# Kernel tuning notes

Hardware: AMD Instinct MI355X
Metric: run time of the kernel (lower is better)

The kernel has to match this reference:

```python
import jax, jax.numpy as jnp
import numpy as np

# --- static config ---
B = 64        # graphs per batch
NPG = 512     # nodes per graph
N = B * NPG   # total nodes = 32768
EPG = 8192    # edges per graph (avg degree 16)
E = B * EPG   # total edges = 524288
L = 16        # tokens per node
V = 50000     # vocab
H = 256       # hidden_size == rnn hidden_size
P = 128       # projection_dim
K1 = 256      # ceil(0.5 * 512) nodes kept after pool 1
K2 = 128      # ceil(0.5 * 256) nodes kept after pool 2
PAD = 0


def setup_inputs() -> dict:
    key = jax.random.key(0)
    ks = jax.random.split(key, 16)
    tokens = jax.random.randint(ks[0], (N, L), 0, V, dtype=jnp.int32)
    eg = jnp.repeat(jnp.arange(B, dtype=jnp.int32), EPG)  # graph id per edge
    src = jax.random.randint(ks[1], (E,), 0, NPG, dtype=jnp.int32) + eg * NPG
    dst = jax.random.randint(ks[2], (E,), 0, NPG, dtype=jnp.int32) + eg * NPG
    edge_attr = jax.random.uniform(ks[3], (E, 2), dtype=jnp.float32)
    sH = 1.0 / np.sqrt(H).astype(np.float32)
    sP = 1.0 / np.sqrt(P).astype(np.float32)
    return {
        'tokens': tokens, 'src': src, 'dst': dst, 'edge_attr': edge_attr,
        'emb': jax.random.normal(ks[4], (V, H), jnp.float32) * 0.05,
        'W0': jax.random.normal(ks[5], (H, H), jnp.float32) * sH,
        'b0': jnp.zeros((H,), jnp.float32),
        'W1': jax.random.normal(ks[6], (H, H), jnp.float32) * sH,
        'b1': jnp.zeros((H,), jnp.float32),
        'p0': jax.random.normal(ks[7], (H,), jnp.float32),
        'p1': jax.random.normal(ks[8], (H,), jnp.float32),
        'wg': jax.random.normal(ks[9], (H, 1), jnp.float32) * sH,
        'bg': jnp.zeros((1,), jnp.float32),
        'Wp1': jax.random.normal(ks[10], (H, P), jnp.float32) * sH,
        'bp1': jnp.zeros((P,), jnp.float32),
        'Wp2': jax.random.normal(ks[11], (P, P), jnp.float32) * sP,
        'bp2': jnp.zeros((P,), jnp.float32),
    }


def _st_encode(tokens, emb):
    # STEncoder proxy: embed token ids, masked mean over non-pad tokens -> [N, H]
    mask = (tokens != PAD).astype(jnp.float32)  # [N, L]
    e = emb[tokens] * mask[..., None]           # [N, L, H]
    cnt = jnp.maximum(mask.sum(-1, keepdims=True), 1.0)
    return e.sum(1) / cnt


def _gcn(x, W, b, src, dst, w, n):
    # GCNConv with edge weights + self loops (fill 1), symmetric normalization
    h = x @ W                                        # [n, H]
    deg = jax.ops.segment_sum(w, dst, num_segments=n) + 1.0
    dinv = jax.lax.rsqrt(deg)
    norm = dinv[src] * w * dinv[dst]                 # [E]
    agg = jax.ops.segment_sum(h[src] * norm[:, None], dst, num_segments=n)
    return agg + h * (1.0 / deg)[:, None] + b


def _topk_pool(x, p, src, dst, w, n_per, k):
    # TopKPooling: score = x.p/||p||, keep top-k per graph, gate by tanh(score)
    G = x.shape[0] // n_per
    score = (x @ p) / jnp.linalg.norm(p)
    vals, idx = jax.lax.top_k(score.reshape(G, n_per), k)   # [G, k]
    perm = (idx + (jnp.arange(G, dtype=jnp.int32) * n_per)[:, None]).reshape(-1)
    x_new = x[perm] * jnp.tanh(vals.reshape(-1))[:, None]
    new_of_old = jnp.full((G * n_per,), -1, jnp.int32).at[perm].set(
        jnp.arange(G * k, dtype=jnp.int32))
    ns, nd = new_of_old[src], new_of_old[dst]
    keep = (ns >= 0) & (nd >= 0)
    # masked edges: weight 0 -> contribute nothing (== subgraph filtering)
    return (x_new, jnp.where(keep, ns, 0), jnp.where(keep, nd, 0),
            jnp.where(keep, w, 0.0))


def _attpool(x, wg, bg, k):
    # GlobalAttention: softmax(Linear(x,1)) over each graph's nodes
    G = x.shape[0] // k
    gate = (x @ wg + bg).reshape(G, k)        # [G, k]
    a = jax.nn.softmax(gate, axis=1)
    return jnp.einsum('gk,gkh->gh', a, x.reshape(G, k, x.shape[-1]))


def reference(tokens, src, dst, edge_attr, emb, W0, b0, W1, b1, p0, p1,
              wg, bg, Wp1, bp1, Wp2, bp2):
    w = edge_attr.mean(axis=1)                 # GCN path: scalar edge weights
    x = _st_encode(tokens, emb)                # [N, H]
    # layer 1
    x = jax.nn.relu(_gcn(x, W0, b0, src, dst, w, N))
    x, src1, dst1, w1 = _topk_pool(x, p0, src, dst, w, NPG, K1)
    out = _attpool(x, wg, bg, K1)              # [B, H]
    # hidden layer
    x = jax.nn.relu(_gcn(x, W1, b1, src1, dst1, w1, B * K1))
    x, _, _, _ = _topk_pool(x, p1, src1, dst1, w1, K1, K2)
    out = out + _attpool(x, wg, bg, K2)
    # projection head + L2 normalize
    h = jax.nn.relu(out @ Wp1 + bp1)
    logits = h @ Wp2 + bp2
    logits = logits / jnp.maximum(
        jnp.linalg.norm(logits, axis=-1, keepdims=True), 1e-12)
    return (logits, out)
```

## Files before the change

kernel.cpp:

```cpp
#include <hip/hip_runtime.h>
#include <hip/hip_bf16.h>

constexpr int C_B   = 64;
constexpr int C_NPG = 512;
constexpr int C_N   = 32768;
constexpr int C_E   = 524288;
constexpr int C_L   = 16;
constexpr int C_H   = 256;
constexpr int C_P   = 128;
constexpr int C_K1  = 256;
constexpr int C_K2  = 128;
constexpr int C_V   = 50000;

typedef __attribute__((ext_vector_type(8)))  short  short8;
typedef __attribute__((ext_vector_type(16))) float  float16;
typedef unsigned short ushort;
typedef unsigned int   uint;

__device__ inline void split_bf16(float x, ushort& h, ushort& l) {
    __hip_bfloat16 bh = __float2bfloat16(x);
    float fh = __bfloat162float(bh);
    __hip_bfloat16 bl = __float2bfloat16(x - fh);
    h = __builtin_bit_cast(ushort, bh);
    l = __builtin_bit_cast(ushort, bl);
}

__device__ inline ushort f2h(float x) {
    return __builtin_bit_cast(ushort, (_Float16)x);
}
__device__ inline float4 h4_to_f4(ushort4 v) {
    return make_float4((float)__builtin_bit_cast(_Float16, v.x),
                       (float)__builtin_bit_cast(_Float16, v.y),
                       (float)__builtin_bit_cast(_Float16, v.z),
                       (float)__builtin_bit_cast(_Float16, v.w));
}

__global__ void k_init(float* __restrict__ degb, int* __restrict__ indegb,
                       float* __restrict__ deg1, int* __restrict__ indeg1,
                       const float* __restrict__ p0, const float* __restrict__ p1,
                       float* __restrict__ invnp) {
    int b = blockIdx.x, t = threadIdx.x;
    if (b < 128)      degb[b * 256 + t] = 0.f;
    else if (b < 256) indegb[(b - 128) * 256 + t] = 0;
    else if (b < 320) deg1[(b - 256) * 256 + t] = 0.f;
    else if (b < 384) indeg1[(b - 320) * 256 + t] = 0;
    else {
        const float* p = (b == 384) ? p0 : p1;
        __shared__ float r[256];
        float v = p[t];
        r[t] = v * v; __syncthreads();
        for (int s = 128; s; s >>= 1) { if (t < s) r[t] += r[t + s]; __syncthreads(); }
        if (t == 0) invnp[b - 384] = rsqrtf(r[0]);
    }
}

__global__ void k_embcvt(const float* __restrict__ emb, ushort* __restrict__ emb16) {
    int i = (blockIdx.x * 256 + threadIdx.x) * 8;
    float4 a = *(const float4*)&emb[i];
    float4 b = *(const float4*)&emb[i + 4];
    short8 o;
    o[0] = (short)f2h(a.x); o[1] = (short)f2h(a.y);
    o[2] = (short)f2h(a.z); o[3] = (short)f2h(a.w);
    o[4] = (short)f2h(b.x); o[5] = (short)f2h(b.y);
    o[6] = (short)f2h(b.z); o[7] = (short)f2h(b.w);
    *(short8*)&emb16[i] = o;
}

__global__ void k_edge_w(const float* __restrict__ ea, const int* __restrict__ dst,
                         float* __restrict__ w, float* __restrict__ deg,
                         int* __restrict__ indeg) {
    int e = blockIdx.x * blockDim.x + threadIdx.x;
    if (e < C_E) {
        float ww = 0.5f * (ea[2 * e] + ea[2 * e + 1]);
        w[e] = ww;
        int d = dst[e];
        atomicAdd(&deg[d], ww);
        atomicAdd(&indeg[d], 1);
    }
}

template <int NPER>
__global__ void k_scan(const int* __restrict__ indeg, int* __restrict__ rowstart,
                       int* __restrict__ cursor, float* __restrict__ deg,
                       float* __restrict__ dinv) {
    int g = blockIdx.x, t = threadIdx.x;
    int node = g * NPER + t;
    float d = deg[node] + 1.f;
    dinv[node] = rsqrtf(d);
    deg[node]  = 1.f / d;
    __shared__ int s[NPER];
    int v = indeg[node];
    s[t] = v;
    __syncthreads();
    for (int off = 1; off < NPER; off <<= 1) {
        int add = (t >= off) ? s[t - off] : 0;
        __syncthreads();
        s[t] += add;
        __syncthreads();
    }
    int start = g * 8192 + s[t] - v;
    rowstart[node] = start;
    cursor[node]   = start;
}

__global__ void k_csr_scatter(const int* __restrict__ src, const int* __restrict__ dst,
                              const float* __restrict__ w, const float* __restrict__ dinv,
                              int* __restrict__ cursor, int* __restrict__ csr_src,
                              float* __restrict__ csr_nrm) {
    int e = blockIdx.x * blockDim.x + threadIdx.x;
    if (e >= C_E) return;
    int s = src[e], d = dst[e];
    int slot = atomicAdd(&cursor[d], 1);
    csr_src[slot] = s;
    csr_nrm[slot] = dinv[s] * w[e] * dinv[d];
}

__global__ void k_csr_scatter2(const int* __restrict__ src1, const int* __restrict__ dst1,
                               const float* __restrict__ w1, const float* __restrict__ dinv,
                               int* __restrict__ cursor, int* __restrict__ csr_src,
                               float* __restrict__ csr_nrm) {
    int e = blockIdx.x * blockDim.x + threadIdx.x;
    if (e >= C_E) return;
    int d = dst1[e];
    if (d < 0) return;
    int s = src1[e];
    int slot = atomicAdd(&cursor[d], 1);
    csr_src[slot] = s;
    csr_nrm[slot] = dinv[s] * w1[e] * dinv[d];
}

__global__ __launch_bounds__(256)
void k_gcn_gather(const ushort* __restrict__ Hm, const int* __restrict__ rowstart,
                  const int* __restrict__ indeg, const int* __restrict__ csr_src,
                  const float* __restrict__ csr_nrm, const float* __restrict__ selfw,
                  const float* __restrict__ bias, const float* __restrict__ p,
                  const float* __restrict__ invnp, float* __restrict__ Xout,
                  float* __restrict__ score, int nnodes) {
    int n    = (blockIdx.x * blockDim.x + threadIdx.x) >> 6;
    int lane = threadIdx.x & 63;
    if (n >= nnodes) return;
    int h4 = lane * 4;
    float4 hv = h4_to_f4(*(const ushort4*)&Hm[(size_t)n * C_H + h4]);
    float  sw = selfw[n];
    float4 bv = *(const float4*)&bias[h4];
    float4 acc = make_float4(fmaf(hv.x, sw, bv.x), fmaf(hv.y, sw, bv.y),
                             fmaf(hv.z, sw, bv.z), fmaf(hv.w, sw, bv.w));
    int start = rowstart[n], cnt = indeg[n];
    const int*   sp = csr_src + start;
    const float* np = csr_nrm + start;
    #pragma unroll 4
    for (int j = 0; j < cnt; ++j) {
        int   s  = sp[j];
        float nm = np[j];
        float4 xv = h4_to_f4(*(const ushort4*)&Hm[(size_t)s * C_H + h4]);
        acc.x = fmaf(nm, xv.x, acc.x);
        acc.y = fmaf(nm, xv.y, acc.y);
        acc.z = fmaf(nm, xv.z, acc.z);
        acc.w = fmaf(nm, xv.w, acc.w);
    }
    acc.x = fmaxf(acc.x, 0.f); acc.y = fmaxf(acc.y, 0.f);
    acc.z = fmaxf(acc.z, 0.f); acc.w = fmaxf(acc.w, 0.f);
    *(float4*)&Xout[(size_t)n * C_H + h4] = acc;
    float4 pv = *(const float4*)&p[h4];
    float s = acc.x * pv.x + acc.y * pv.y + acc.z * pv.z + acc.w * pv.w;
    #pragma unroll
    for (int m = 32; m; m >>= 1) s += __shfl_xor(s, m, 64);
    if (lane == 0) score[n] = s * invnp[0];
}

__device__ inline void emit_frags(const float* Xs, ushort* __restrict__ outh,
                                  ushort* __restrict__ outl, int mtg, int tid) {
    #pragma unroll
    for (int i = 0; i < 4; ++i) {
        int c    = tid + 256 * i;
        int kst  = c >> 6;
        int lane = c & 63;
        int ml   = lane & 31;
        int kb   = kst * 16 + (lane >> 5) * 8;
        short8 hv, lv;
        #pragma unroll
        for (int j = 0; j < 8; ++j) {
            ushort h, l;
            split_bf16(Xs[ml * 257 + kb + j], h, l);
            hv[j] = (short)h; lv[j] = (short)l;
        }
        size_t base = (size_t)mtg * 8192 + (size_t)c * 8;
        *(short8*)&outh[base] = hv;
        *(short8*)&outl[base] = lv;
    }
}

__global__ __launch_bounds__(256)
void k_st_encode4(const int* __restrict__ tokens, const ushort* __restrict__ emb16,
                  ushort* __restrict__ Xh, ushort* __restrict__ Xl) {
    __shared__ float Xs[32 * 257];
    __shared__ int tokS[512];
    int tid = threadIdx.x;
    int blk = blockIdx.x;
    tokS[tid]       = tokens[(size_t)blk * 512 + tid];
    tokS[tid + 256] = tokens[(size_t)blk * 512 + tid + 256];
    __syncthreads();
    int w    = tid >> 6;
    int lane = tid & 63;
    for (int i = 0; i < 8; ++i) {
        int nl = w * 8 + i;
        float4 acc = make_float4(0.f, 0.f, 0.f, 0.f);
        int cnt = 0;
        #pragma unroll
        for (int t = 0; t < C_L; ++t) {
            int tk = tokS[nl * 16 + t];
            if (tk != 0) {
                float4 ev = h4_to_f4(*(const ushort4*)&emb16[(size_t)tk * C_H + lane * 4]);
                acc.x += ev.x; acc.y += ev.y; acc.z += ev.z; acc.w += ev.w;
                cnt++;
            }
        }
        float inv = 1.f / fmaxf((float)cnt, 1.f);
        float* xr = &Xs[nl * 257 + lane * 4];
        xr[0] = acc.x * inv; xr[1] = acc.y * inv;
        xr[2] = acc.z * inv; xr[3] = acc.w * inv;
    }
    __syncthreads();
    emit_frags(Xs, Xh, Xl, blk, tid);
}

__global__ void k_wprep(const float* __restrict__ W0, const float* __restrict__ W1,
                        ushort* __restrict__ W0h, ushort* __restrict__ W0l,
                        ushort* __restrict__ W1h, ushort* __restrict__ W1l) {
    int g = blockIdx.x * blockDim.x + threadIdx.x;
    int which = g >> 16;
    int idx = g & 65535;
    int k = idx >> 8, n = idx & 255;
    float x = (which ? W1 : W0)[idx];
    ushort h, l;
    split_bf16(x, h, l);
    size_t a = ((size_t)(n >> 5) * 16 + (k >> 4)) * 512 + ((k >> 3) & 1) * 256
             + (n & 31) * 8 + (k & 7);
    if (which) { W1h[a] = h; W1l[a] = l; }
    else       { W0h[a] = h; W0l[a] = l; }
}

__global__ __launch_bounds__(256)
void k_gemm_mfma(const ushort* __restrict__ Ah, const ushort* __restrict__ Al,
                 const ushort* __restrict__ Bh, const ushort* __restrict__ Bl,
                 ushort* __restrict__ C) {
    __shared__ short lds[16384];
    int tid  = threadIdx.x;
    int lane = tid & 63;
    int wid  = tid >> 6;
    int wm   = wid & 1, wn = wid >> 1;
    int mb   = blockIdx.x;
    int nb   = blockIdx.y;

    float16 acc[2][2];
    #pragma unroll
    for (int mi = 0; mi < 2; ++mi)
        #pragma unroll
        for (int ni = 0; ni < 2; ++ni)
            #pragma unroll
            for (int r = 0; r < 16; ++r) acc[mi][ni][r] = 0.f;

    for (int kc = 0; kc < 8; ++kc) {
        __syncthreads();
        #pragma unroll
        for (int i = 0; i < 4; ++i) {
            int a  = tid + 256 * i;
            int s  = a >> 9;
            int mt = (a >> 7) & 3;
            int k2 = (a >> 6) & 1;
            int ln = a & 63;
            const ushort* ap = (s ? Al : Ah)
                + (((size_t)(mb * 4 + mt) * 16 + kc * 2 + k2) * 64 + ln) * 8;
            *(int4*)&lds[a * 8] = *(const int4*)ap;
            const ushort* bp = (s ? Bl : Bh)
                + (((size_t)(nb * 4 + mt) * 16 + kc * 2 + k2) * 64 + ln) * 8;
            *(int4*)&lds[8192 + a * 8] = *(const int4*)bp;
        }
        __syncthreads();
        #pragma unroll
        for (int k2 = 0; k2 < 2; ++k2) {
            short8 ah[2], al[2], bh[2], bl[2];
            #pragma unroll
            for (int mi = 0; mi < 2; ++mi) {
                int mt = wm * 2 + mi;
                ah[mi] = *(short8*)&lds[((mt * 2 + k2) * 64 + lane) * 8];
                al[mi] = *(short8*)&lds[(((4 + mt) * 2 + k2) * 64 + lane) * 8];
            }
            #pragma unroll
            for (int ni = 0; ni < 2; ++ni) {
                int nt = wn * 2 + ni;
                bh[ni] = *(short8*)&lds[8192 + ((nt * 2 + k2) * 64 + lane) * 8];
                bl[ni] = *(short8*)&lds[8192 + (((4 + nt) * 2 + k2) * 64 + lane) * 8];
            }
            #pragma unroll
            for (int mi = 0; mi < 2; ++mi)
                #pragma unroll
                for (int ni = 0; ni < 2; ++ni) {
                    acc[mi][ni] = __builtin_amdgcn_mfma_f32_32x32x16_bf16(
                        ah[mi], bh[ni], acc[mi][ni], 0, 0, 0);
                    acc[mi][ni] = __builtin_amdgcn_mfma_f32_32x32x16_bf16(
                        ah[mi], bl[ni], acc[mi][ni], 0, 0, 0);
                    acc[mi][ni] = __builtin_amdgcn_mfma_f32_32x32x16_bf16(
                        al[mi], bh[ni], acc[mi][ni], 0, 0, 0);
                }
        }
    }
    int col = lane & 31;
    int rquad = 4 * (lane >> 5);
    #pragma unroll
    for (int mi = 0; mi < 2; ++mi)
        #pragma unroll
        for (int ni = 0; ni < 2; ++ni) {
            int mbase = mb * 128 + wm * 64 + mi * 32;
            int nbase = nb * 128 + wn * 64 + ni * 32 + col;
            #pragma unroll
            for (int r = 0; r < 16; ++r) {
                int row = (r & 3) + 8 * (r >> 2) + rquad;
                C[(size_t)(mbase + row) * C_H + nbase] = f2h(acc[mi][ni][r]);
            }
        }
}

template <int NPER, int KKEEP>
__global__ void k_pool(const float* __restrict__ score, int* __restrict__ new_of_old,
                       int* __restrict__ old_of_new, float* __restrict__ gate) {
    int g = blockIdx.x;
    int t = threadIdx.x;
    __shared__ float sv[NPER];
    __shared__ int   si[NPER];
    sv[t] = score[g * NPER + t];
    si[t] = t;
    __syncthreads();
    for (int k = 2; k <= NPER; k <<= 1) {
        for (int j = k >> 1; j > 0; j >>= 1) {
            int ixj = t ^ j;
            if (ixj > t) {
                bool desc = ((t & k) == 0);
                float a = sv[t], b = sv[ixj];
                bool sw = desc ? (a < b) : (a > b);
                if (sw) {
                    sv[t] = b; sv[ixj] = a;
                    int tmp = si[t]; si[t] = si[ixj]; si[ixj] = tmp;
                }
            }
            __syncthreads();
        }
    }
    int old_global = g * NPER + si[t];
    if (t < KKEEP) {
        new_of_old[old_global]    = g * KKEEP + t;
        old_of_new[g * KKEEP + t] = old_global;
        gate[g * KKEEP + t]       = tanhf(sv[t]);
    } else {
        new_of_old[old_global] = -1;
    }
}

__global__ __launch_bounds__(256)
void k_gather32(const float* __restrict__ X, const int* __restrict__ old_of_new,
                const float* __restrict__ gate, float* __restrict__ Xn,
                ushort* __restrict__ Xnh, ushort* __restrict__ Xnl) {
    __shared__ float Xs[32 * 257];
    __shared__ int   olds[32];
    __shared__ float gts[32];
    int tid = threadIdx.x;
    int blk = blockIdx.x;
    if (tid < 32) {
        olds[tid] = old_of_new[blk * 32 + tid];
        gts[tid]  = gate[blk * 32 + tid];
    }
    __syncthreads();
    #pragma unroll
    for (int i = 0; i < 8; ++i) {
        int u  = tid + 256 * i;
        int nl = u >> 6;
        int c4 = (u & 63) * 4;
        float4 v = *(const float4*)&X[(size_t)olds[nl] * C_H + c4];
        float g = gts[nl];
        v.x *= g; v.y *= g; v.z *= g; v.w *= g;
        *(float4*)&Xn[((size_t)blk * 32 + nl) * C_H + c4] = v;
        float* xr = &Xs[nl * 257 + c4];
        xr[0] = v.x; xr[1] = v.y; xr[2] = v.z; xr[3] = v.w;
    }
    __syncthreads();
    emit_frags(Xs, Xnh, Xnl, blk, tid);
}

__global__ void k_remap(const int* __restrict__ src, const int* __restrict__ dst,
                        const float* __restrict__ w, const int* __restrict__ noo,
                        int* __restrict__ src1, int* __restrict__ dst1,
                        float* __restrict__ w1, float* __restrict__ deg1,
                        int* __restrict__ indeg1) {
    int e = blockIdx.x * blockDim.x + threadIdx.x;
    if (e >= C_E) return;
    int ns = noo[src[e]], nd = noo[dst[e]];
    bool keep = (ns >= 0) && (nd >= 0);
    src1[e] = ns;
    dst1[e] = keep ? nd : -1;
    w1[e]   = w[e];
    if (keep) {
        atomicAdd(&deg1[nd], w[e]);
        atomicAdd(&indeg1[nd], 1);
    }
}

template <int KN, bool ACC>
__global__ void k_attpool(const float* __restrict__ X, const float* __restrict__ wg,
                          const float* __restrict__ bg, float* __restrict__ out) {
    int g = blockIdx.x;
    int t = threadIdx.x;
    __shared__ float sa[KN];
    __shared__ float red[KN];
    const float* xr = &X[(size_t)(g * KN + t) * C_H];
    float dt = 0.f;
    for (int k = 0; k < C_H; k += 4) {
        float4 wv = *(const float4*)&wg[k];
        float4 xv = *(const float4*)&xr[k];
        dt += wv.x * xv.x + wv.y * xv.y + wv.z * xv.z + wv.w * xv.w;
    }
    dt += bg[0];
    red[t] = dt; __syncthreads();
    for (int s = KN / 2; s > 0; s >>= 1) { if (t < s) red[t] = fmaxf(red[t], red[t + s]); __syncthreads(); }
    float mx = red[0]; __syncthreads();
    float ex = expf(dt - mx);
    red[t] = ex; __syncthreads();
    for (int s = KN / 2; s > 0; s >>= 1) { if (t < s) red[t] += red[t + s]; __syncthreads(); }
    float inv = 1.f / red[0];
    sa[t] = ex * inv;
    __syncthreads();
    for (int h = t; h < C_H; h += KN) {
        float acc = 0.f;
        for (int n = 0; n < KN; ++n) acc += sa[n] * X[(size_t)(g * KN + n) * C_H + h];
        if (ACC) out[g * C_H + h] += acc; else out[g * C_H + h] = acc;
    }
}

__global__ __launch_bounds__(128)
void k_pool2_att(const float* __restrict__ X, const int* __restrict__ oon2,
                 const float* __restrict__ gate2, const float* __restrict__ wg,
                 const float* __restrict__ bg, float* __restrict__ outb) {
    int g = blockIdx.x;
    int t = threadIdx.x;
    __shared__ int   rows[C_K2];
    __shared__ float gt[C_K2];
    __shared__ float sd[C_K2];
    __shared__ float sa[C_K2];
    __shared__ float red[C_K2];
    rows[t] = oon2[g * C_K2 + t];
    gt[t]   = gate2[g * C_K2 + t];
    __syncthreads();
    int wv = t >> 6, lane = t & 63;
    float4 wv4 = *(const float4*)&wg[lane * 4];
    for (int idx = wv; idx < C_K2; idx += 2) {
        float4 xv = *(const float4*)&X[(size_t)rows[idx] * C_H + lane * 4];
        float s = xv.x * wv4.x + xv.y * wv4.y + xv.z * wv4.z + xv.w * wv4.w;
        #pragma unroll
        for (int m = 32; m; m >>= 1) s += __shfl_xor(s, m, 64);
        if (lane == 0) sd[idx] = gt[idx] * s + bg[0];
    }
    __syncthreads();
    red[t] = sd[t]; __syncthreads();
    for (int s = 64; s; s >>= 1) { if (t < s) red[t] = fmaxf(red[t], red[t + s]); __syncthreads(); }
    float mx = red[0]; __syncthreads();
    float ex = expf(sd[t] - mx);
    red[t] = ex; __syncthreads();
    for (int s = 64; s; s >>= 1) { if (t < s) red[t] += red[t + s]; __syncthreads(); }
    sa[t] = ex / red[0];
    __syncthreads();
    float acc0 = 0.f, acc1 = 0.f;
    for (int n = 0; n < C_K2; ++n) {
        float an = sa[n] * gt[n];
        const float* xr = &X[(size_t)rows[n] * C_H];
        acc0 = fmaf(an, xr[t], acc0);
        acc1 = fmaf(an, xr[t + 128], acc1);
    }
    outb[g * C_H + t]       += acc0;
    outb[g * C_H + t + 128] += acc1;
}

__global__ void k_head(const float* __restrict__ outb, const float* __restrict__ Wp1,
                       const float* __restrict__ bp1, const float* __restrict__ Wp2,
                       const float* __restrict__ bp2, float* __restrict__ dout) {
    int g = blockIdx.x;
    int t = threadIdx.x;
    __shared__ float so[C_H];
    so[t] = outb[g * C_H + t];
    so[t + 128] = outb[g * C_H + t + 128];
    __syncthreads();
    float acc = bp1[t];
    for (int k = 0; k < C_H; ++k) acc += so[k] * Wp1[k * C_P + t];
    float hv = fmaxf(acc, 0.f);
    __shared__ float sh[C_P];
    sh[t] = hv; __syncthreads();
    float lg = bp2[t];
    for (int k = 0; k < C_P; ++k) lg += sh[k] * Wp2[k * C_P + t];
    __shared__ float red[C_P];
    red[t] = lg * lg; __syncthreads();
    for (int s = 64; s > 0; s >>= 1) { if (t < s) red[t] += red[t + s]; __syncthreads(); }
    float nrm = fmaxf(sqrtf(red[0]), 1e-12f);
    dout[g * C_P + t] = lg / nrm;
    dout[C_B * C_P + g * C_H + t]       = so[t];
    dout[C_B * C_P + g * C_H + t + 128] = so[t + 128];
}

extern "C" void kernel_launch(void* const* d_in, const int* in_sizes, int n_in,
                              void* d_out, int out_size, void* d_ws, size_t ws_size,
                              hipStream_t stream) {
    const int*   tokens = (const int*)d_in[0];
    const int*   src    = (const int*)d_in[1];
    const int*   dst    = (const int*)d_in[2];
    const float* eattr  = (const float*)d_in[3];
    const float* emb    = (const float*)d_in[4];
    const float* W0     = (const float*)d_in[5];
    const float* b0     = (const float*)d_in[6];
    const float* W1     = (const float*)d_in[7];
    const float* b1     = (const float*)d_in[8];
    const float* p0     = (const float*)d_in[9];
    const float* p1     = (const float*)d_in[10];
    const float* wg     = (const float*)d_in[11];
    const float* bg     = (const float*)d_in[12];
    const float* Wp1    = (const float*)d_in[13];
    const float* bp1    = (const float*)d_in[14];
    const float* Wp2    = (const float*)d_in[15];
    const float* bp2    = (const float*)d_in[16];
    float* out = (float*)d_out;

    float* f = (float*)d_ws;
    size_t o = 0;
    float*  XB    = f + o; o += (size_t)C_N * C_H;
    float*  HB    = f + o; o += (size_t)C_N * C_H;
    ushort* XFh   = (ushort*)(f + o); o += (size_t)C_N * C_H / 2;
    ushort* XFl   = (ushort*)(f + o); o += (size_t)C_N * C_H / 2;
    float*  wbuf  = f + o; o += C_E;
    float*  degb  = f + o; o += C_N;
    float*  dinv  = f + o; o += C_N;
    int*    indegb= (int*)(f + o); o += C_N;
    int*    rowst = (int*)(f + o); o += C_N;
    int*    curs  = (int*)(f + o); o += C_N;
    int*    csrs  = (int*)(f + o); o += C_E;
    float*  csrn  = f + o; o += C_E;
    int*    noo   = (int*)(f + o); o += C_N;
    int*    oon   = (int*)(f + o); o += C_B * C_K1;
    float*  gate1 = f + o; o += C_B * C_K1;
    int*    src1  = (int*)(f + o); o += C_E;
    int*    dst1  = (int*)(f + o); o += C_E;
    float*  w1    = f + o; o += C_E;
    float*  deg1  = f + o; o += C_B * C_K1;
    int*    indeg1= (int*)(f + o); o += C_B * C_K1;
    int*    rowst1= (int*)(f + o); o += C_B * C_K1;
    int*    curs1 = (int*)(f + o); o += C_B * C_K1;
    int*    oon2  = (int*)(f + o); o += C_B * C_K2;
    float*  gate2 = f + o; o += C_B * C_K2;
    float*  outb  = f + o; o += C_B * C_H;
    float*  score = f + o; o += C_N;
    float*  invnp = f + o; o += 16;
    ushort* W0h   = (ushort*)(f + o); o += C_H * C_H / 2;
    ushort* W0l   = (ushort*)(f + o); o += C_H * C_H / 2;
    ushort* W1h   = (ushort*)(f + o); o += C_H * C_H / 2;
    ushort* W1l   = (ushort*)(f + o); o += C_H * C_H / 2;

    ushort* emb16 = (ushort*)XB;
    float*  AGG1  = XB;
    float*  x1    = HB;
    ushort* Hhf   = (ushort*)(HB + (size_t)C_N * C_H / 2);

    k_init<<<386, 256, 0, stream>>>(degb, indegb, deg1, indeg1, p0, p1, invnp);
    k_embcvt<<<(C_V * C_H) / 2048, 256, 0, stream>>>(emb, emb16);
    k_edge_w<<<C_E / 256, 256, 0, stream>>>(eattr, dst, wbuf, degb, indegb);
    k_wprep<<<131072 / 256, 256, 0, stream>>>(W0, W1, W0h, W0l, W1h, W1l);
    k_st_encode4<<<C_N / 32, 256, 0, stream>>>(tokens, emb16, XFh, XFl);
    k_scan<C_NPG><<<C_B, C_NPG, 0, stream>>>(indegb, rowst, curs, degb, dinv);
    k_csr_scatter<<<C_E / 256, 256, 0, stream>>>(src, dst, wbuf, dinv, curs, csrs, csrn);

    k_gemm_mfma<<<dim3(C_N / 128, 2), 256, 0, stream>>>(XFh, XFl, W0h, W0l, Hhf);
    k_gcn_gather<<<(C_N * 64) / 256, 256, 0, stream>>>(
        Hhf, rowst, indegb, csrs, csrn, degb, b0, p0, invnp, XB, score, C_N);

    k_pool<C_NPG, C_K1><<<C_B, C_NPG, 0, stream>>>(score, noo, oon, gate1);
    k_gather32<<<(C_B * C_K1) / 32, 256, 0, stream>>>(XB, oon, gate1, x1, XFh, XFl);
    k_remap<<<C_E / 256, 256, 0, stream>>>(src, dst, wbuf, noo, src1, dst1, w1, deg1, indeg1);
    k_attpool<C_K1, false><<<C_B, C_K1, 0, stream>>>(x1, wg, bg, outb);

    k_gemm_mfma<<<dim3((C_B * C_K1) / 128, 2), 256, 0, stream>>>(XFh, XFl, W1h, W1l, Hhf);
    k_scan<C_K1><<<C_B, C_K1, 0, stream>>>(indeg1, rowst1, curs1, deg1, dinv);
    k_csr_scatter2<<<C_E / 256, 256, 0, stream>>>(src1, dst1, w1, dinv, curs1, csrs, csrn);
    k_gcn_gather<<<(C_B * C_K1 * 64) / 256, 256, 0, stream>>>(
        Hhf, rowst1, indeg1, csrs, csrn, deg1, b1, p1, invnp + 1, AGG1, score, C_B * C_K1);

    k_pool<C_K1, C_K2><<<C_B, C_K1, 0, stream>>>(score, noo, oon2, gate2);
    k_pool2_att<<<C_B, C_K2, 0, stream>>>(AGG1, oon2, gate2, wg, bg, outb);

    k_head<<<C_B, C_P, 0, stream>>>(outb, Wp1, bp1, Wp2, bp2, out);
}
```

Baseline: 431.4 us.

## Fuse pooling, edge remap and CSR build into per-graph kernels

Merges the setup kernels (embedding convert, edge weights, weight prep, p-norm) into one launch and replaces zero-init with a memset. Replaces the first top-k pool, gather, remap, attention pool, scan and CSR scatter with one per-graph block that uses shared-memory atomics and a local scan. The second pool and attention are also fused into one kernel. This removes many launches and global intermediates (src1/dst1/w1, noo/oon). The cost is that the fused stages now run on only 64 blocks, which limits parallelism on the heavy per-graph work.

```diff
diff --git a/kernel.cpp b/kernel.cpp
--- a/kernel.cpp
+++ b/kernel.cpp
@@ -35,47 +35,51 @@
                        (float)__builtin_bit_cast(_Float16, v.w));
 }
 
-__global__ void k_init(float* __restrict__ degb, int* __restrict__ indegb,
-                       float* __restrict__ deg1, int* __restrict__ indeg1,
-                       const float* __restrict__ p0, const float* __restrict__ p1,
-                       float* __restrict__ invnp) {
+__global__ void k_pre(const float* __restrict__ emb, ushort* __restrict__ emb16,
+                      const float* __restrict__ ea, const int* __restrict__ dst,
+                      float* __restrict__ w, float* __restrict__ degb, int* __restrict__ indegb,
+                      const float* __restrict__ W0, const float* __restrict__ W1,
+                      ushort* __restrict__ W0h, ushort* __restrict__ W0l,
+                      ushort* __restrict__ W1h, ushort* __restrict__ W1l,
+                      const float* __restrict__ p0, const float* __restrict__ p1,
+                      float* __restrict__ invnp) {
     int b = blockIdx.x, t = threadIdx.x;
-    if (b < 128)      degb[b * 256 + t] = 0.f;
-    else if (b < 256) indegb[(b - 128) * 256 + t] = 0;
-    else if (b < 320) deg1[(b - 256) * 256 + t] = 0.f;
-    else if (b < 384) indeg1[(b - 320) * 256 + t] = 0;
-    else {
-        const float* p = (b == 384) ? p0 : p1;
-        __shared__ float r[256];
+    __shared__ float r[256];
+    if (b < 6250) {
+        int i = (b * 256 + t) * 8;
+        float4 a = *(const float4*)&emb[i];
+        float4 c = *(const float4*)&emb[i + 4];
+        short8 o;
+        o[0] = (short)f2h(a.x); o[1] = (short)f2h(a.y);
+        o[2] = (short)f2h(a.z); o[3] = (short)f2h(a.w);
+        o[4] = (short)f2h(c.x); o[5] = (short)f2h(c.y);
+        o[6] = (short)f2h(c.z); o[7] = (short)f2h(c.w);
+        *(short8*)&emb16[i] = o;
+    } else if (b < 8298) {
+        int e = (b - 6250) * 256 + t;
+        float ww = 0.5f * (ea[2 * e] + ea[2 * e + 1]);
+        w[e] = ww;
+        int d = dst[e];
+        atomicAdd(&degb[d], ww);
+        atomicAdd(&indegb[d], 1);
+    } else if (b < 8810) {
+        int g = (b - 8298) * 256 + t;
+        int which = g >> 16;
+        int idx = g & 65535;
+        int k = idx >> 8, n = idx & 255;
+        float x = (which ? W1 : W0)[idx];
+        ushort h, l;
+        split_bf16(x, h, l);
+        size_t a = ((size_t)(n >> 5) * 16 + (k >> 4)) * 512 + ((k >> 3) & 1) * 256
+                 + (n & 31) * 8 + (k & 7);
+        if (which) { W1h[a] = h; W1l[a] = l; }
+        else       { W0h[a] = h; W0l[a] = l; }
+    } else {
+        const float* p = (b == 8810) ? p0 : p1;
         float v = p[t];
         r[t] = v * v; __syncthreads();
         for (int s = 128; s; s >>= 1) { if (t < s) r[t] += r[t + s]; __syncthreads(); }
-        if (t == 0) invnp[b - 384] = rsqrtf(r[0]);
-    }
-}
-
-__global__ void k_embcvt(const float* __restrict__ emb, ushort* __restrict__ emb16) {
-    int i = (blockIdx.x * 256 + threadIdx.x) * 8;
-    float4 a = *(const float4*)&emb[i];
-    float4 b = *(const float4*)&emb[i + 4];
-    short8 o;
-    o[0] = (short)f2h(a.x); o[1] = (short)f2h(a.y);
-    o[2] = (short)f2h(a.z); o[3] = (short)f2h(a.w);
-    o[4] = (short)f2h(b.x); o[5] = (short)f2h(b.y);
-    o[6] = (short)f2h(b.z); o[7] = (short)f2h(b.w);
-    *(short8*)&emb16[i] = o;
-}
-
-__global__ void k_edge_w(const float* __restrict__ ea, const int* __restrict__ dst,
-                         float* __restrict__ w, float* __restrict__ deg,
-                         int* __restrict__ indeg) {
-    int e = blockIdx.x * blockDim.x + threadIdx.x;
-    if (e < C_E) {
-        float ww = 0.5f * (ea[2 * e] + ea[2 * e + 1]);
-        w[e] = ww;
-        int d = dst[e];
-        atomicAdd(&deg[d], ww);
-        atomicAdd(&indeg[d], 1);
+        if (t == 0) invnp[b - 8810] = rsqrtf(r[0]);
     }
 }
 
@@ -113,20 +117,6 @@
     int slot = atomicAdd(&cursor[d], 1);
     csr_src[slot] = s;
     csr_nrm[slot] = dinv[s] * w[e] * dinv[d];
-}
-
-__global__ void k_csr_scatter2(const int* __restrict__ src1, const int* __restrict__ dst1,
-                               const float* __restrict__ w1, const float* __restrict__ dinv,
-                               int* __restrict__ cursor, int* __restrict__ csr_src,
-                               float* __restrict__ csr_nrm) {
-    int e = blockIdx.x * blockDim.x + threadIdx.x;
-    if (e >= C_E) return;
-    int d = dst1[e];
-    if (d < 0) return;
-    int s = src1[e];
-    int slot = atomicAdd(&cursor[d], 1);
-    csr_src[slot] = s;
-    csr_nrm[slot] = dinv[s] * w1[e] * dinv[d];
 }
 
 __global__ __launch_bounds__(256)
@@ -168,28 +158,6 @@
     if (lane == 0) score[n] = s * invnp[0];
 }
 
-__device__ inline void emit_frags(const float* Xs, ushort* __restrict__ outh,
-                                  ushort* __restrict__ outl, int mtg, int tid) {
-    #pragma unroll
-    for (int i = 0; i < 4; ++i) {
-        int c    = tid + 256 * i;
-        int kst  = c >> 6;
-        int lane = c & 63;
-        int ml   = lane & 31;
-        int kb   = kst * 16 + (lane >> 5) * 8;
-        short8 hv, lv;
-        #pragma unroll
-        for (int j = 0; j < 8; ++j) {
-            ushort h, l;
-            split_bf16(Xs[ml * 257 + kb + j], h, l);
-            hv[j] = (short)h; lv[j] = (short)l;
-        }
-        size_t base = (size_t)mtg * 8192 + (size_t)c * 8;
-        *(short8*)&outh[base] = hv;
-        *(short8*)&outl[base] = lv;
-    }
-}
-
 __global__ __launch_bounds__(256)
 void k_st_encode4(const int* __restrict__ tokens, const ushort* __restrict__ emb16,
                   ushort* __restrict__ Xh, ushort* __restrict__ Xl) {
@@ -221,23 +189,24 @@
         xr[2] = acc.z * inv; xr[3] = acc.w * inv;
     }
     __syncthreads();
-    emit_frags(Xs, Xh, Xl, blk, tid);
-}
-
-__global__ void k_wprep(const float* __restrict__ W0, const float* __restrict__ W1,
-                        ushort* __restrict__ W0h, ushort* __restrict__ W0l,
-                        ushort* __restrict__ W1h, ushort* __restrict__ W1l) {
-    int g = blockIdx.x * blockDim.x + threadIdx.x;
-    int which = g >> 16;
-    int idx = g & 65535;
-    int k = idx >> 8, n = idx & 255;
-    float x = (which ? W1 : W0)[idx];
-    ushort h, l;
-    split_bf16(x, h, l);
-    size_t a = ((size_t)(n >> 5) * 16 + (k >> 4)) * 512 + ((k >> 3) & 1) * 256
-             + (n & 31) * 8 + (k & 7);
-    if (which) { W1h[a] = h; W1l[a] = l; }
-    else       { W0h[a] = h; W0l[a] = l; }
+    #pragma unroll
+    for (int i = 0; i < 4; ++i) {
+        int c    = tid + 256 * i;
+        int kst  = c >> 6;
+        int ln   = c & 63;
+        int ml   = ln & 31;
+        int kb   = kst * 16 + (ln >> 5) * 8;
+        short8 hv, lv;
+        #pragma unroll
+        for (int j = 0; j < 8; ++j) {
+            ushort h, l;
+            split_bf16(Xs[ml * 257 + kb + j], h, l);
+            hv[j] = (short)h; lv[j] = (short)l;
+        }
+        size_t base = (size_t)blk * 8192 + (size_t)c * 8;
+        *(short8*)&Xh[base] = hv;
+        *(short8*)&Xl[base] = lv;
+    }
 }
 
 __global__ __launch_bounds__(256)
@@ -321,161 +290,221 @@
         }
 }
 
-template <int NPER, int KKEEP>
-__global__ void k_pool(const float* __restrict__ score, int* __restrict__ new_of_old,
-                       int* __restrict__ old_of_new, float* __restrict__ gate) {
-    int g = blockIdx.x;
-    int t = threadIdx.x;
-    __shared__ float sv[NPER];
-    __shared__ int   si[NPER];
-    sv[t] = score[g * NPER + t];
+__global__ __launch_bounds__(512)
+void k_pool1_fused(const float* __restrict__ score, const float* __restrict__ X,
+                   const int* __restrict__ src, const int* __restrict__ dst,
+                   const float* __restrict__ wbuf,
+                   const float* __restrict__ wg, const float* __restrict__ bg,
+                   ushort* __restrict__ XFh, ushort* __restrict__ XFl,
+                   float* __restrict__ outb,
+                   float* __restrict__ selfw1, int* __restrict__ rowst1,
+                   int* __restrict__ indeg1, int* __restrict__ csrs,
+                   float* __restrict__ csrn) {
+    int g = blockIdx.x, t = threadIdx.x;
+    __shared__ float sv[C_NPG];
+    __shared__ int   si[C_NPG];
+    __shared__ int   nooL[C_NPG];
+    __shared__ int   olds[C_K1];
+    __shared__ float gt[C_K1];
+    __shared__ float sd[C_K1];
+    __shared__ float red[C_K1];
+    __shared__ float an[C_K1];
+    __shared__ float Xs[32 * 257];
+    __shared__ int   indegL[C_K1];
+    __shared__ float degL[C_K1];
+    __shared__ float dinvL[C_K1];
+    __shared__ int   rowstL[C_K1];
+    __shared__ int   cursL[C_K1];
+
+    sv[t] = score[g * C_NPG + t];
     si[t] = t;
     __syncthreads();
-    for (int k = 2; k <= NPER; k <<= 1) {
+    for (int k = 2; k <= C_NPG; k <<= 1)
         for (int j = k >> 1; j > 0; j >>= 1) {
             int ixj = t ^ j;
             if (ixj > t) {
                 bool desc = ((t & k) == 0);
                 float a = sv[t], b = sv[ixj];
-                bool sw = desc ? (a < b) : (a > b);
-                if (sw) {
+                if (desc ? (a < b) : (a > b)) {
                     sv[t] = b; sv[ixj] = a;
                     int tmp = si[t]; si[t] = si[ixj]; si[ixj] = tmp;
                 }
             }
             __syncthreads();
         }
-    }
-    int old_global = g * NPER + si[t];
-    if (t < KKEEP) {
-        new_of_old[old_global]    = g * KKEEP + t;
-        old_of_new[g * KKEEP + t] = old_global;
-        gate[g * KKEEP + t]       = tanhf(sv[t]);
-    } else {
-        new_of_old[old_global] = -1;
+    nooL[si[t]] = (t < C_K1) ? t : -1;
+    if (t < C_K1) {
+        olds[t]   = si[t];
+        gt[t]     = tanhf(sv[t]);
+        indegL[t] = 0;
+        degL[t]   = 0.f;
+    }
+    __syncthreads();
+
+    int w = t >> 6, lane = t & 63;
+    float4 wg4 = *(const float4*)&wg[lane * 4];
+    float bgv = bg[0];
+    for (int r = w; r < C_K1; r += 8) {
+        float4 xv = *(const float4*)&X[(size_t)(g * C_NPG + olds[r]) * C_H + lane * 4];
+        float s = xv.x * wg4.x + xv.y * wg4.y + xv.z * wg4.z + xv.w * wg4.w;
+        #pragma unroll
+        for (int m = 32; m; m >>= 1) s += __shfl_xor(s, m, 64);
+        if (lane == 0) sd[r] = gt[r] * s + bgv;
+    }
+    __syncthreads();
+    if (t < C_K1) red[t] = sd[t];
+    __syncthreads();
+    for (int s = 128; s; s >>= 1) { if (t < s) red[t] = fmaxf(red[t], red[t + s]); __syncthreads(); }
+    float mx = red[0];
+    __syncthreads();
+    if (t < C_K1) { float ex = expf(sd[t] - mx); an[t] = ex; red[t] = ex; }
+    __syncthreads();
+    for (int s = 128; s; s >>= 1) { if (t < s) red[t] += red[t + s]; __syncthreads(); }
+    if (t < C_K1) an[t] = an[t] / red[0] * gt[t];
+    __syncthreads();
+    {
+        int h = t & 255, half = t >> 8;
+        float acc = 0.f;
+        for (int n = half * 128; n < half * 128 + 128; ++n)
+            acc = fmaf(an[n], X[(size_t)(g * C_NPG + olds[n]) * C_H + h], acc);
+        __syncthreads();
+        if (half == 1) sd[h] = acc;
+        __syncthreads();
+        if (half == 0) outb[g * C_H + h] = acc + sd[h];
+    }
+    __syncthreads();
+
+    for (int c = 0; c < 8; ++c) {
+        #pragma unroll
+        for (int i = 0; i < 4; ++i) {
+            int u  = t + 512 * i;
+            int nl = u >> 6, ln = u & 63;
+            int r  = c * 32 + nl;
+            float4 v = *(const float4*)&X[(size_t)(g * C_NPG + olds[r]) * C_H + ln * 4];
+            float gg = gt[r];
+            float* xr = &Xs[nl * 257 + ln * 4];
+            xr[0] = v.x * gg; xr[1] = v.y * gg; xr[2] = v.z * gg; xr[3] = v.w * gg;
+        }
+        __syncthreads();
+        #pragma unroll
+        for (int i = 0; i < 2; ++i) {
+            int cch = t + 512 * i;
+            int kst = cch >> 6, ln = cch & 63;
+            int ml  = ln & 31;
+            int kb  = kst * 16 + (ln >> 5) * 8;
+            short8 hv, lv;
+            #pragma unroll
+            for (int j = 0; j < 8; ++j) {
+                ushort h, l;
+                split_bf16(Xs[ml * 257 + kb + j], h, l);
+                hv[j] = (short)h; lv[j] = (short)l;
+            }
+            size_t base = (size_t)(g * 8 + c) * 8192 + (size_t)cch * 8;
+            *(short8*)&XFh[base] = hv;
+            *(short8*)&XFl[base] = lv;
+        }
+        __syncthreads();
+    }
+
+    for (int i = 0; i < 16; ++i) {
+        int e  = g * 8192 + t + 512 * i;
+        int ns = nooL[src[e] - g * C_NPG];
+        int nd = nooL[dst[e] - g * C_NPG];
+        if (ns >= 0 && nd >= 0) {
+            atomicAdd(&indegL[nd], 1);
+            unsafeAtomicAdd(&degL[nd], wbuf[e]);
+        }
+    }
+    __syncthreads();
+    if (t < C_K1) {
+        float d = degL[t] + 1.f;
+        dinvL[t] = rsqrtf(d);
+        selfw1[g * C_K1 + t] = 1.f / d;
+        indeg1[g * C_K1 + t] = indegL[t];
+        rowstL[t] = indegL[t];
+    }
+    __syncthreads();
+    for (int off = 1; off < C_K1; off <<= 1) {
+        int add = 0;
+        if (t < C_K1 && t >= off) add = rowstL[t - off];
+        __syncthreads();
+        if (t < C_K1) rowstL[t] += add;
+        __syncthreads();
+    }
+    if (t < C_K1) {
+        int start = g * 8192 + rowstL[t] - indegL[t];
+        rowstL[t] = start;
+        cursL[t]  = start;
+        rowst1[g * C_K1 + t] = start;
+    }
+    __syncthreads();
+    for (int i = 0; i < 16; ++i) {
+        int e  = g * 8192 + t + 512 * i;
+        int ns = nooL[src[e] - g * C_NPG];
+        int nd = nooL[dst[e] - g * C_NPG];
+        if (ns >= 0 && nd >= 0) {
+            int slot = atomicAdd(&cursL[nd], 1);
+            csrs[slot] = g * C_K1 + ns;
+            csrn[slot] = dinvL[ns] * wbuf[e] * dinvL[nd];
+        }
     }
 }
 
 __global__ __launch_bounds__(256)
-void k_gather32(const float* __restrict__ X, const int* __restrict__ old_of_new,
-                const float* __restrict__ gate, float* __restrict__ Xn,
-                ushort* __restrict__ Xnh, ushort* __restrict__ Xnl) {
-    __shared__ float Xs[32 * 257];
-    __shared__ int   olds[32];
-    __shared__ float gts[32];
-    int tid = threadIdx.x;
-    int blk = blockIdx.x;
-    if (tid < 32) {
-        olds[tid] = old_of_new[blk * 32 + tid];
-        gts[tid]  = gate[blk * 32 + tid];
-    }
-    __syncthreads();
-    #pragma unroll
-    for (int i = 0; i < 8; ++i) {
-        int u  = tid + 256 * i;
-        int nl = u >> 6;
-        int c4 = (u & 63) * 4;
-        float4 v = *(const float4*)&X[(size_t)olds[nl] * C_H + c4];
-        float g = gts[nl];
-        v.x *= g; v.y *= g; v.z *= g; v.w *= g;
-        *(float4*)&Xn[((size_t)blk * 32 + nl) * C_H + c4] = v;
-        float* xr = &Xs[nl * 257 + c4];
-        xr[0] = v.x; xr[1] = v.y; xr[2] = v.z; xr[3] = v.w;
-    }
-    __syncthreads();
-    emit_frags(Xs, Xnh, Xnl, blk, tid);
-}
-
-__global__ void k_remap(const int* __restrict__ src, const int* __restrict__ dst,
-                        const float* __restrict__ w, const int* __restrict__ noo,
-                        int* __restrict__ src1, int* __restrict__ dst1,
-                        float* __restrict__ w1, float* __restrict__ deg1,
-                        int* __restrict__ indeg1) {
-    int e = blockIdx.x * blockDim.x + threadIdx.x;
-    if (e >= C_E) return;
-    int ns = noo[src[e]], nd = noo[dst[e]];
-    bool keep = (ns >= 0) && (nd >= 0);
-    src1[e] = ns;
-    dst1[e] = keep ? nd : -1;
-    w1[e]   = w[e];
-    if (keep) {
-        atomicAdd(&deg1[nd], w[e]);
-        atomicAdd(&indeg1[nd], 1);
-    }
-}
-
-template <int KN, bool ACC>
-__global__ void k_attpool(const float* __restrict__ X, const float* __restrict__ wg,
-                          const float* __restrict__ bg, float* __restrict__ out) {
-    int g = blockIdx.x;
-    int t = threadIdx.x;
-    __shared__ float sa[KN];
-    __shared__ float red[KN];
-    const float* xr = &X[(size_t)(g * KN + t) * C_H];
-    float dt = 0.f;
-    for (int k = 0; k < C_H; k += 4) {
-        float4 wv = *(const float4*)&wg[k];
-        float4 xv = *(const float4*)&xr[k];
-        dt += wv.x * xv.x + wv.y * xv.y + wv.z * xv.z + wv.w * xv.w;
-    }
-    dt += bg[0];
-    red[t] = dt; __syncthreads();
-    for (int s = KN / 2; s > 0; s >>= 1) { if (t < s) red[t] = fmaxf(red[t], red[t + s]); __syncthreads(); }
-    float mx = red[0]; __syncthreads();
-    float ex = expf(dt - mx);
-    red[t] = ex; __syncthreads();
-    for (int s = KN / 2; s > 0; s >>= 1) { if (t < s) red[t] += red[t + s]; __syncthreads(); }
-    float inv = 1.f / red[0];
-    sa[t] = ex * inv;
-    __syncthreads();
-    for (int h = t; h < C_H; h += KN) {
-        float acc = 0.f;
-        for (int n = 0; n < KN; ++n) acc += sa[n] * X[(size_t)(g * KN + n) * C_H + h];
-        if (ACC) out[g * C_H + h] += acc; else out[g * C_H + h] = acc;
-    }
-}
-
-__global__ __launch_bounds__(128)
-void k_pool2_att(const float* __restrict__ X, const int* __restrict__ oon2,
-                 const float* __restrict__ gate2, const float* __restrict__ wg,
-                 const float* __restrict__ bg, float* __restrict__ outb) {
-    int g = blockIdx.x;
-    int t = threadIdx.x;
-    __shared__ int   rows[C_K2];
+void k_pool2_fused(const float* __restrict__ score, const float* __restrict__ X,
+                   const float* __restrict__ wg, const float* __restrict__ bg,
+                   float* __restrict__ outb) {
+    int g = blockIdx.x, t = threadIdx.x;
+    __shared__ float sv[C_K1];
+    __shared__ int   si[C_K1];
+    __shared__ int   olds[C_K2];
     __shared__ float gt[C_K2];
     __shared__ float sd[C_K2];
-    __shared__ float sa[C_K2];
     __shared__ float red[C_K2];
-    rows[t] = oon2[g * C_K2 + t];
-    gt[t]   = gate2[g * C_K2 + t];
-    __syncthreads();
-    int wv = t >> 6, lane = t & 63;
-    float4 wv4 = *(const float4*)&wg[lane * 4];
-    for (int idx = wv; idx < C_K2; idx += 2) {
-        float4 xv = *(const float4*)&X[(size_t)rows[idx] * C_H + lane * 4];
-        float s = xv.x * wv4.x + xv.y * wv4.y + xv.z * wv4.z + xv.w * wv4.w;
+    __shared__ float an[C_K2];
+    sv[t] = score[g * C_K1 + t];
+    si[t] = t;
+    __syncthreads();
+    for (int k = 2; k <= C_K1; k <<= 1)
+        for (int j = k >> 1; j > 0; j >>= 1) {
+            int ixj = t ^ j;
+            if (ixj > t) {
+                bool desc = ((t & k) == 0);
+                float a = sv[t], b = sv[ixj];
+                if (desc ? (a < b) : (a > b)) {
+                    sv[t] = b; sv[ixj] = a;
+                    int tmp = si[t]; si[t] = si[ixj]; si[ixj] = tmp;
+                }
+            }
+            __syncthreads();
+        }
+    if (t < C_K2) { olds[t] = si[t]; gt[t] = tanhf(sv[t]); }
+    __syncthreads();
+    int w = t >> 6, lane = t & 63;
+    float4 wg4 = *(const float4*)&wg[lane * 4];
+    float bgv = bg[0];
+    for (int r = w; r < C_K2; r += 4) {
+        float4 xv = *(const float4*)&X[(size_t)(g * C_K1 + olds[r]) * C_H + lane * 4];
+        float s = xv.x * wg4.x + xv.y * wg4.y + xv.z * wg4.z + xv.w * wg4.w;
         #pragma unroll
         for (int m = 32; m; m >>= 1) s += __shfl_xor(s, m, 64);
-        if (lane == 0) sd[idx] = gt[idx] * s + bg[0];
-    }
-    __syncthreads();
-    red[t] = sd[t]; __syncthreads();
+        if (lane == 0) sd[r] = gt[r] * s + bgv;
+    }
+    __syncthreads();
+    if (t < C_K2) red[t] = sd[t];
+    __syncthreads();
     for (int s = 64; s; s >>= 1) { if (t < s) red[t] = fmaxf(red[t], red[t + s]); __syncthreads(); }
-    float mx = red[0]; __syncthreads();
-    float ex = expf(sd[t] - mx);
-    red[t] = ex; __syncthreads();
+    float mx = red[0];
+    __syncthreads();
+    if (t < C_K2) { float ex = expf(sd[t] - mx); an[t] = ex; red[t] = ex; }
+    __syncthreads();
     for (int s = 64; s; s >>= 1) { if (t < s) red[t] += red[t + s]; __syncthreads(); }
-    sa[t] = ex / red[0];
-    __syncthreads();
-    float acc0 = 0.f, acc1 = 0.f;
-    for (int n = 0; n < C_K2; ++n) {
-        float an = sa[n] * gt[n];
-        const float* xr = &X[(size_t)rows[n] * C_H];
-        acc0 = fmaf(an, xr[t], acc0);
-        acc1 = fmaf(an, xr[t + 128], acc1);
-    }
-    outb[g * C_H + t]       += acc0;
-    outb[g * C_H + t + 128] += acc1;
+    if (t < C_K2) an[t] = an[t] / red[0] * gt[t];
+    __syncthreads();
+    float acc = 0.f;
+    for (int n = 0; n < C_K2; ++n)
+        acc = fmaf(an[n], X[(size_t)(g * C_K1 + olds[n]) * C_H + t], acc);
+    outb[g * C_H + t] += acc;
 }
 
 __global__ void k_head(const float* __restrict__ outb, const float* __restrict__ Wp1,
@@ -533,24 +562,15 @@
     ushort* XFl   = (ushort*)(f + o); o += (size_t)C_N * C_H / 2;
     float*  wbuf  = f + o; o += C_E;
     float*  degb  = f + o; o += C_N;
+    int*    indegb= (int*)(f + o); o += C_N;
     float*  dinv  = f + o; o += C_N;
-    int*    indegb= (int*)(f + o); o += C_N;
     int*    rowst = (int*)(f + o); o += C_N;
     int*    curs  = (int*)(f + o); o += C_N;
     int*    csrs  = (int*)(f + o); o += C_E;
     float*  csrn  = f + o; o += C_E;
-    int*    noo   = (int*)(f + o); o += C_N;
-    int*    oon   = (int*)(f + o); o += C_B * C_K1;
-    float*  gate1 = f + o; o += C_B * C_K1;
-    int*    src1  = (int*)(f + o); o += C_E;
-    int*    dst1  = (int*)(f + o); o += C_E;
-    float*  w1    = f + o; o += C_E;
     float*  deg1  = f + o; o += C_B * C_K1;
     int*    indeg1= (int*)(f + o); o += C_B * C_K1;
     int*    rowst1= (int*)(f + o); o += C_B * C_K1;
-    int*    curs1 = (int*)(f + o); o += C_B * C_K1;
-    int*    oon2  = (int*)(f + o); o += C_B * C_K2;
-    float*  gate2 = f + o; o += C_B * C_K2;
     float*  outb  = f + o; o += C_B * C_H;
     float*  score = f + o; o += C_N;
     float*  invnp = f + o; o += 16;
@@ -561,13 +581,12 @@
 
     ushort* emb16 = (ushort*)XB;
     float*  AGG1  = XB;
-    float*  x1    = HB;
-    ushort* Hhf   = (ushort*)(HB + (size_t)C_N * C_H / 2);
-
-    k_init<<<386, 256, 0, stream>>>(degb, indegb, deg1, indeg1, p0, p1, invnp);
-    k_embcvt<<<(C_V * C_H) / 2048, 256, 0, stream>>>(emb, emb16);
-    k_edge_w<<<C_E / 256, 256, 0, stream>>>(eattr, dst, wbuf, degb, indegb);
-    k_wprep<<<131072 / 256, 256, 0, stream>>>(W0, W1, W0h, W0l, W1h, W1l);
+    ushort* Hhf   = (ushort*)HB;
+
+    hipMemsetAsync(degb, 0, 2 * C_N * sizeof(float), stream);
+
+    k_pre<<<8812, 256, 0, stream>>>(emb, emb16, eattr, dst, wbuf, degb, indegb,
+                                    W0, W1, W0h, W0l, W1h, W1l, p0, p1, invnp);
     k_st_encode4<<<C_N / 32, 256, 0, stream>>>(tokens, emb16, XFh, XFl);
     k_scan<C_NPG><<<C_B, C_NPG, 0, stream>>>(indegb, rowst, curs, degb, dinv);
     k_csr_scatter<<<C_E / 256, 256, 0, stream>>>(src, dst, wbuf, dinv, curs, csrs, csrn);
@@ -576,19 +595,15 @@
     k_gcn_gather<<<(C_N * 64) / 256, 256, 0, stream>>>(
         Hhf, rowst, indegb, csrs, csrn, degb, b0, p0, invnp, XB, score, C_N);
 
-    k_pool<C_NPG, C_K1><<<C_B, C_NPG, 0, stream>>>(score, noo, oon, gate1);
-    k_gather32<<<(C_B * C_K1) / 32, 256, 0, stream>>>(XB, oon, gate1, x1, XFh, XFl);
-    k_remap<<<C_E / 256, 256, 0, stream>>>(src, dst, wbuf, noo, src1, dst1, w1, deg1, indeg1);
-    k_attpool<C_K1, false><<<C_B, C_K1, 0, stream>>>(x1, wg, bg, outb);
+    k_pool1_fused<<<C_B, 512, 0, stream>>>(
+        score, XB, src, dst, wbuf, wg, bg, XFh, XFl, outb,
+        deg1, rowst1, indeg1, csrs, csrn);
 
     k_gemm_mfma<<<dim3((C_B * C_K1) / 128, 2), 256, 0, stream>>>(XFh, XFl, W1h, W1l, Hhf);
-    k_scan<C_K1><<<C_B, C_K1, 0, stream>>>(indeg1, rowst1, curs1, deg1, dinv);
-    k_csr_scatter2<<<C_E / 256, 256, 0, stream>>>(src1, dst1, w1, dinv, curs1, csrs, csrn);
     k_gcn_gather<<<(C_B * C_K1 * 64) / 256, 256, 0, stream>>>(
         Hhf, rowst1, indeg1, csrs, csrn, deg1, b1, p1, invnp + 1, AGG1, score, C_B * C_K1);
 
-    k_pool<C_K1, C_K2><<<C_B, C_K1, 0, stream>>>(score, noo, oon2, gate2);
-    k_pool2_att<<<C_B, C_K2, 0, stream>>>(AGG1, oon2, gate2, wg, bg, outb);
+    k_pool2_fused<<<C_B, C_K1, 0, stream>>>(score, AGG1, wg, bg, outb);
 
     k_head<<<C_B, C_P, 0, stream>>>(outb, Wp1, bp1, Wp2, bp2, out);
 }
```

New measurement: 405.7 us. 6.0% less time.
